# Kernel optimization log

Measured on AMD Instinct MI355X. Metric: run time of the kernel, lower is better.

The kernel has to match this reference:

```python
import jax, jax.numpy as jnp
import numpy as np

N_NODES = 100000
N_EDGES = 1600000
IN_DIM = 128
HID_DIM = 128


def setup_inputs() -> dict:
    key = jax.random.key(0)
    k_x, k_e, k_w1, k_w2, k_b1, k_b2 = jax.random.split(key, 6)
    x = jax.random.normal(k_x, (N_NODES, IN_DIM), dtype=jnp.float32)
    edge_index = jax.random.randint(k_e, (2, N_EDGES), 0, N_NODES, dtype=jnp.int64)
    # GCNConv params: linear weight (no bias in lin), plus post-aggregation bias
    s1 = 1.0 / np.sqrt(IN_DIM)
    s2 = 1.0 / np.sqrt(HID_DIM)
    W1 = jax.random.uniform(k_w1, (IN_DIM, HID_DIM), jnp.float32, -s1, s1)
    b1 = jnp.zeros((HID_DIM,), jnp.float32)
    W2 = jax.random.uniform(k_w2, (HID_DIM, HID_DIM), jnp.float32, -s2, s2)
    b2 = jnp.zeros((HID_DIM,), jnp.float32)
    return {"x": x, "edge_index": edge_index, "W1": W1, "b1": b1, "W2": W2, "b2": b2}


def _gcn_conv(x, row, col, norm, W, b, n_nodes):
    # h = x W ; out[col] += norm * h[row] ; + b   (PyG GCNConv math)
    h = x @ W
    msg = h[row] * norm[:, None]          # [E+N, H] edge-gathered messages
    out = jax.ops.segment_sum(msg, col, num_segments=n_nodes)
    return out + b


def reference(x, edge_index, W1, b1, W2, b2):
    n = x.shape[0]
    # add self-loops (PyG gcn_norm default: add_self_loops=True, edge_weight=1)
    loop = jnp.arange(n, dtype=edge_index.dtype)
    row = jnp.concatenate([edge_index[0], loop])
    col = jnp.concatenate([edge_index[1], loop])
    # symmetric normalization: deg computed at col (target)
    deg = jax.ops.segment_sum(jnp.ones(row.shape[0], x.dtype), col, num_segments=n)
    dis = jnp.where(deg > 0, jax.lax.rsqrt(jnp.maximum(deg, 1e-30)), 0.0)
    norm = dis[row] * dis[col]            # [E+N]
    h = _gcn_conv(x, row, col, norm, W1, b1, n)
    h = jax.nn.relu(h)
    out = _gcn_conv(h, row, col, norm, W2, b2, n)
    return out
```

## Files before the change

kernel.cpp:

```cpp
#include <hip/hip_runtime.h>

#define NN 100000
#define NE 1600000
#define FD 128
#define NBUK 196
#define BCAP 9216
#define EPBB 8192
#define NBB 196
#define NGROUP 6250

typedef unsigned int  u32;
typedef unsigned short u16;
typedef __bf16 bf16x8 __attribute__((ext_vector_type(8)));
typedef float  f32x4v __attribute__((ext_vector_type(4)));

__device__ __forceinline__ u16 f2bf(float f) {
    u32 u = __float_as_uint(f);
    u32 r = (u + 0x7FFFu + ((u >> 16) & 1u)) >> 16;
    return (u16)r;
}

__device__ __forceinline__ void acc2(float& x, float& y, float wt, u32 w) {
    x += wt * __uint_as_float(w << 16);
    y += wt * __uint_as_float(w & 0xffff0000u);
}
__device__ __forceinline__ void acc8(float4& L, float4& H, float wt, uint4 u) {
    acc2(L.x, L.y, wt, u.x); acc2(L.z, L.w, wt, u.y);
    acc2(H.x, H.y, wt, u.z); acc2(H.z, H.w, wt, u.w);
}


__global__ void k_binit(int* __restrict__ bcur) {
    int i = threadIdx.x;
    if (i < NBUK) bcur[i] = i * BCAP;
}

__global__ __launch_bounds__(256) void k_bin(const int* __restrict__ row,
                                             const int* __restrict__ col,
                                             int* __restrict__ bcur,
                                             u32* __restrict__ ebuf) {
    __shared__ int hist[NBUK];
    const int tid = threadIdx.x;
    for (int i = tid; i < NBUK; i += 256) hist[i] = 0;
    __syncthreads();
    const int e0 = blockIdx.x * EPBB;
    const int e1 = min(e0 + EPBB, NE);
    for (int e = e0 + tid; e < e1; e += 256)
        atomicAdd(&hist[col[e] >> 9], 1);
    __syncthreads();
    for (int i = tid; i < NBUK; i += 256) {
        int c = hist[i];
        hist[i] = c ? atomicAdd(&bcur[i], c) : 0;
    }
    __syncthreads();
    for (int e = e0 + tid; e < e1; e += 256) {
        int c = col[e];
        int pos = atomicAdd(&hist[c >> 9], 1);
        ebuf[pos] = ((u32)row[e] << 9) | (u32)(c & 511);
    }
}

__global__ __launch_bounds__(256) void k_bucket(const u32* __restrict__ ebuf,
                                                const int* __restrict__ bcur,
                                                int* __restrict__ nstart,
                                                int* __restrict__ ndeg,
                                                float* __restrict__ dis,
                                                int* __restrict__ srcs) {
    __shared__ int lcnt[512];
    __shared__ int s[256];
    const int tid = threadIdx.x;
    const int b = blockIdx.x;
    const int base = b * BCAP;
    const int end = bcur[b];

    lcnt[tid] = 0; lcnt[tid + 256] = 0;
    __syncthreads();
    for (int i = base + tid; i < end; i += 256)
        atomicAdd(&lcnt[ebuf[i] & 511], 1);
    __syncthreads();

    const int c0 = lcnt[tid * 2], c1 = lcnt[tid * 2 + 1];
    s[tid] = c0 + c1;
    __syncthreads();
    for (int off = 1; off < 256; off <<= 1) {
        int t = 0;
        if (tid >= off) t = s[tid - off];
        __syncthreads();
        if (tid >= off) s[tid] += t;
        __syncthreads();
    }
    const int excl = (tid == 0) ? 0 : s[tid - 1];
    __syncthreads();
    lcnt[tid * 2] = excl;
    lcnt[tid * 2 + 1] = excl + c0;

    const int v0 = b * 512 + tid * 2;
    if (v0 < NN) {
        nstart[v0] = base + excl;
        ndeg[v0] = c0;
        dis[v0] = rsqrtf((float)c0 + 1.0f);
    }
    if (v0 + 1 < NN) {
        nstart[v0 + 1] = base + excl + c0;
        ndeg[v0 + 1] = c1;
        dis[v0 + 1] = rsqrtf((float)c1 + 1.0f);
    }
    __syncthreads();

    for (int i = base + tid; i < end; i += 256) {
        u32 p = ebuf[i];
        int pos = atomicAdd(&lcnt[p & 511], 1);
        srcs[base + pos] = (int)(p >> 9);
    }
}

__global__ __launch_bounds__(256) void k_wts(const int* __restrict__ nstart,
                                             const int* __restrict__ ndeg,
                                             const float* __restrict__ dis,
                                             const int* __restrict__ srcs,
                                             int2* __restrict__ ew) {
    const int v = (blockIdx.x * 256 + threadIdx.x) >> 4;
    if (v >= NN) return;
    const int l = threadIdx.x & 15;
    const float dv = dis[v];
    const int s0 = nstart[v], d = ndeg[v];
    for (int e = s0 + l; e < s0 + d; e += 16) {
        int s = srcs[e];
        ew[e] = make_int2(s, __float_as_int(dv * dis[s]));
    }
}

__global__ void k_packW2(const float* __restrict__ W1, const float* __restrict__ W2,
                         u16* __restrict__ Wf1, u16* __restrict__ Wf2) {
    int tid = blockIdx.x * 256 + threadIdx.x;
    if (tid >= 2048) return;
    int l = tid & 63;
    int tq = tid >> 6;
    int q = tq & 3, t = tq >> 2;
    int n = t * 16 + (l & 15);
    int k0 = q * 32 + (l >> 4) * 8;
    u32 p[4], r[4];
    for (int jj = 0; jj < 4; ++jj) {
        u16 lo1 = f2bf(W1[(size_t)(k0 + 2 * jj) * FD + n]);
        u16 hi1 = f2bf(W1[(size_t)(k0 + 2 * jj + 1) * FD + n]);
        p[jj] = (u32)lo1 | ((u32)hi1 << 16);
        u16 lo2 = f2bf(W2[(size_t)(k0 + 2 * jj) * FD + n]);
        u16 hi2 = f2bf(W2[(size_t)(k0 + 2 * jj + 1) * FD + n]);
        r[jj] = (u32)lo2 | ((u32)hi2 << 16);
    }
    *(uint4*)&Wf1[(size_t)tid * 8] = make_uint4(p[0], p[1], p[2], p[3]);
    *(uint4*)&Wf2[(size_t)tid * 8] = make_uint4(r[0], r[1], r[2], r[3]);
}

template <bool F32IN>
__global__ __launch_bounds__(256, 4) void k_gemm_mfma(const void* __restrict__ inv,
                                                      const u16* __restrict__ Wf,
                                                      u16* __restrict__ out) {
    __shared__ u16 Wl[16384];
    const int tid = threadIdx.x;
    {
        const uint4* s = (const uint4*)Wf;
        uint4* d = (uint4*)Wl;
#pragma unroll
        for (int i = 0; i < 8; ++i) d[tid + 256 * i] = s[tid + 256 * i];
    }
    __syncthreads();

    const int wave = tid >> 6, lane = tid & 63;
    const int gid = blockIdx.x * 4 + wave;
    if (gid >= NGROUP) return;
    const int row0 = gid * 16;
    const int lr = lane & 15;
    const int lh = lane >> 4;

    f32x4v acc[8];
#pragma unroll
    for (int t = 0; t < 8; ++t) { f32x4v z = {0.f, 0.f, 0.f, 0.f}; acc[t] = z; }

#pragma unroll
    for (int q = 0; q < 4; ++q) {
        bf16x8 a;
        if (F32IN) {
            const float* arow = (const float*)inv + (size_t)(row0 + lr) * FD + lh * 8 + q * 32;
            float4 f0 = *(const float4*)(arow);
            float4 f1 = *(const float4*)(arow + 4);
            union { bf16x8 v; u16 s[8]; } ua;
            ua.s[0] = f2bf(f0.x); ua.s[1] = f2bf(f0.y);
            ua.s[2] = f2bf(f0.z); ua.s[3] = f2bf(f0.w);
            ua.s[4] = f2bf(f1.x); ua.s[5] = f2bf(f1.y);
            ua.s[6] = f2bf(f1.z); ua.s[7] = f2bf(f1.w);
            a = ua.v;
        } else {
            const u16* arow = (const u16*)inv + (size_t)(row0 + lr) * FD + lh * 8 + q * 32;
            a = *(const bf16x8*)arow;
        }
#pragma unroll
        for (int t = 0; t < 8; ++t) {
            bf16x8 bfr = *(const bf16x8*)(&Wl[(size_t)(t * 4 + q) * 512 + lane * 8]);
            acc[t] = __builtin_amdgcn_mfma_f32_16x16x32_bf16(a, bfr, acc[t], 0, 0, 0);
        }
    }
#pragma unroll
    for (int t = 0; t < 8; ++t) {
#pragma unroll
        for (int j = 0; j < 4; ++j) {
            const int r = row0 + lh * 4 + j;
            out[(size_t)r * FD + t * 16 + lr] = f2bf(acc[t][j]);
        }
    }
}

template <bool BF16OUT>
__global__ __launch_bounds__(256) void k_agg_gather(const u16* __restrict__ hb,
                                                    const float* __restrict__ b,
                                                    const float* __restrict__ dis,
                                                    const int* __restrict__ nstart,
                                                    const int* __restrict__ ndeg,
                                                    const int2* __restrict__ ew,
                                                    void* __restrict__ outv) {
    const int v = (blockIdx.x * 256 + threadIdx.x) >> 4;
    if (v >= NN) return;
    const int f8 = threadIdx.x & 15;
    const uint4* h4 = (const uint4*)hb;

    const float dv = dis[v];
    float4 aL = ((const float4*)b)[f8 * 2];
    float4 aH = ((const float4*)b)[f8 * 2 + 1];
    {
        const float sl = dv * dv;
        uint4 u = h4[(size_t)v * 16 + f8];
        acc8(aL, aH, sl, u);
    }

    int e = nstart[v];
    const int end = e + ndeg[v];
    for (; e + 3 < end; e += 4) {
        const int2 p0 = ew[e], p1 = ew[e + 1], p2 = ew[e + 2], p3 = ew[e + 3];
        const uint4 u0 = h4[(size_t)p0.x * 16 + f8];
        const uint4 u1 = h4[(size_t)p1.x * 16 + f8];
        const uint4 u2 = h4[(size_t)p2.x * 16 + f8];
        const uint4 u3 = h4[(size_t)p3.x * 16 + f8];
        acc8(aL, aH, __int_as_float(p0.y), u0);
        acc8(aL, aH, __int_as_float(p1.y), u1);
        acc8(aL, aH, __int_as_float(p2.y), u2);
        acc8(aL, aH, __int_as_float(p3.y), u3);
    }
    for (; e < end; ++e) {
        const int2 p0 = ew[e];
        const uint4 u0 = h4[(size_t)p0.x * 16 + f8];
        acc8(aL, aH, __int_as_float(p0.y), u0);
    }

    if (BF16OUT) {
        uint4 p;
        p.x = (u32)f2bf(fmaxf(aL.x, 0.f)) | ((u32)f2bf(fmaxf(aL.y, 0.f)) << 16);
        p.y = (u32)f2bf(fmaxf(aL.z, 0.f)) | ((u32)f2bf(fmaxf(aL.w, 0.f)) << 16);
        p.z = (u32)f2bf(fmaxf(aH.x, 0.f)) | ((u32)f2bf(fmaxf(aH.y, 0.f)) << 16);
        p.w = (u32)f2bf(fmaxf(aH.z, 0.f)) | ((u32)f2bf(fmaxf(aH.w, 0.f)) << 16);
        ((uint4*)outv)[(size_t)v * 16 + f8] = p;
    } else {
        float4* o = (float4*)outv;
        o[(size_t)v * 32 + f8 * 2] = aL;
        o[(size_t)v * 32 + f8 * 2 + 1] = aH;
    }
}


extern "C" void kernel_launch(void* const* d_in, const int* in_sizes, int n_in,
                              void* d_out, int out_size, void* d_ws, size_t ws_size,
                              hipStream_t stream) {
    const float* x  = (const float*)d_in[0];
    const int*   ei = (const int*)d_in[1];
    const float* W1 = (const float*)d_in[2];
    const float* b1 = (const float*)d_in[3];
    const float* W2 = (const float*)d_in[4];
    const float* b2 = (const float*)d_in[5];
    float* out = (float*)d_out;

    const int* row = ei;
    const int* col = ei + NE;

    char* base = (char*)d_ws;
    size_t o = 0;
    auto take = [&](size_t bytes) -> void* {
        void* p = base + o;
        o += (bytes + 255) & ~(size_t)255;
        return p;
    };
    int*   nstart  = (int*)take((size_t)NN * 4);
    int*   ndeg    = (int*)take((size_t)NN * 4);
    int*   bcur    = (int*)take(256 * 4);
    float* dis     = (float*)take((size_t)NN * 4);
    u16*   Wf1     = (u16*)take(16384 * 2);
    u16*   Wf2     = (u16*)take(16384 * 2);
    u16*   hb      = (u16*)take((size_t)NN * FD * 2);
    u16*   aggb    = (u16*)take((size_t)NN * FD * 2);
    int*   srcs    = (int*)take((size_t)NBUK * BCAP * 4);
    int2*  ew      = (int2*)take((size_t)NBUK * BCAP * 8);
    u32*   ebuf    = (u32*)take((size_t)NBUK * BCAP * 4);

    k_binit<<<1, 256, 0, stream>>>(bcur);
    k_bin<<<NBB, 256, 0, stream>>>(row, col, bcur, ebuf);
    k_bucket<<<NBUK, 256, 0, stream>>>(ebuf, bcur, nstart, ndeg, dis, srcs);
    k_wts<<<NGROUP, 256, 0, stream>>>(nstart, ndeg, dis, srcs, ew);

    k_packW2<<<8, 256, 0, stream>>>(W1, W2, Wf1, Wf2);

    k_gemm_mfma<true><<<(NGROUP + 3) / 4, 256, 0, stream>>>(x, Wf1, hb);
    k_agg_gather<true><<<NN * 16 / 256, 256, 0, stream>>>(hb, b1, dis, nstart, ndeg, ew, aggb);
    k_gemm_mfma<false><<<(NGROUP + 3) / 4, 256, 0, stream>>>(aggb, Wf2, hb);
    k_agg_gather<false><<<NN * 16 / 256, 256, 0, stream>>>(hb, b2, dis, nstart, ndeg, ew, out);
}
```

Before: 229.7 us.

## Fuse graph binning with first GEMM, fuse layer-1 aggregation with second GEMM

Merges edge binning and the first X·W1 MFMA GEMM into a single launch, with the two roles picked by block index so that they overlap. Fuses the first aggregation (with ReLU) and the second GEMM through a shared-memory tile, which removes the aggb round trip and a separate launch. It also drops the precomputed edge-weight array and instead computes dv*dis[s] inside the gather loops, and merges bcur init with weight packing. Launch count falls from 9 to 5, at the cost of extra dis gathers per edge and W2 fragments read from global memory by every block.

Result: faster. 198.6 us (-13.5%).

```diff
diff --git a/kernel.cpp b/kernel.cpp
--- a/kernel.cpp
+++ b/kernel.cpp
@@ -8,6 +8,7 @@
 #define EPBB 8192
 #define NBB 196
 #define NGROUP 6250
+#define GEMM_BLKS 1563
 
 typedef unsigned int  u32;
 typedef unsigned short u16;
@@ -29,110 +30,14 @@
     acc2(H.x, H.y, wt, u.z); acc2(H.z, H.w, wt, u.w);
 }
 
-
-__global__ void k_binit(int* __restrict__ bcur) {
-    int i = threadIdx.x;
-    if (i < NBUK) bcur[i] = i * BCAP;
-}
-
-__global__ __launch_bounds__(256) void k_bin(const int* __restrict__ row,
-                                             const int* __restrict__ col,
-                                             int* __restrict__ bcur,
-                                             u32* __restrict__ ebuf) {
-    __shared__ int hist[NBUK];
-    const int tid = threadIdx.x;
-    for (int i = tid; i < NBUK; i += 256) hist[i] = 0;
-    __syncthreads();
-    const int e0 = blockIdx.x * EPBB;
-    const int e1 = min(e0 + EPBB, NE);
-    for (int e = e0 + tid; e < e1; e += 256)
-        atomicAdd(&hist[col[e] >> 9], 1);
-    __syncthreads();
-    for (int i = tid; i < NBUK; i += 256) {
-        int c = hist[i];
-        hist[i] = c ? atomicAdd(&bcur[i], c) : 0;
-    }
-    __syncthreads();
-    for (int e = e0 + tid; e < e1; e += 256) {
-        int c = col[e];
-        int pos = atomicAdd(&hist[c >> 9], 1);
-        ebuf[pos] = ((u32)row[e] << 9) | (u32)(c & 511);
-    }
-}
-
-__global__ __launch_bounds__(256) void k_bucket(const u32* __restrict__ ebuf,
-                                                const int* __restrict__ bcur,
-                                                int* __restrict__ nstart,
-                                                int* __restrict__ ndeg,
-                                                float* __restrict__ dis,
-                                                int* __restrict__ srcs) {
-    __shared__ int lcnt[512];
-    __shared__ int s[256];
-    const int tid = threadIdx.x;
-    const int b = blockIdx.x;
-    const int base = b * BCAP;
-    const int end = bcur[b];
-
-    lcnt[tid] = 0; lcnt[tid + 256] = 0;
-    __syncthreads();
-    for (int i = base + tid; i < end; i += 256)
-        atomicAdd(&lcnt[ebuf[i] & 511], 1);
-    __syncthreads();
-
-    const int c0 = lcnt[tid * 2], c1 = lcnt[tid * 2 + 1];
-    s[tid] = c0 + c1;
-    __syncthreads();
-    for (int off = 1; off < 256; off <<= 1) {
-        int t = 0;
-        if (tid >= off) t = s[tid - off];
-        __syncthreads();
-        if (tid >= off) s[tid] += t;
-        __syncthreads();
-    }
-    const int excl = (tid == 0) ? 0 : s[tid - 1];
-    __syncthreads();
-    lcnt[tid * 2] = excl;
-    lcnt[tid * 2 + 1] = excl + c0;
-
-    const int v0 = b * 512 + tid * 2;
-    if (v0 < NN) {
-        nstart[v0] = base + excl;
-        ndeg[v0] = c0;
-        dis[v0] = rsqrtf((float)c0 + 1.0f);
-    }
-    if (v0 + 1 < NN) {
-        nstart[v0 + 1] = base + excl + c0;
-        ndeg[v0 + 1] = c1;
-        dis[v0 + 1] = rsqrtf((float)c1 + 1.0f);
-    }
-    __syncthreads();
-
-    for (int i = base + tid; i < end; i += 256) {
-        u32 p = ebuf[i];
-        int pos = atomicAdd(&lcnt[p & 511], 1);
-        srcs[base + pos] = (int)(p >> 9);
-    }
-}
-
-__global__ __launch_bounds__(256) void k_wts(const int* __restrict__ nstart,
-                                             const int* __restrict__ ndeg,
-                                             const float* __restrict__ dis,
-                                             const int* __restrict__ srcs,
-                                             int2* __restrict__ ew) {
-    const int v = (blockIdx.x * 256 + threadIdx.x) >> 4;
-    if (v >= NN) return;
-    const int l = threadIdx.x & 15;
-    const float dv = dis[v];
-    const int s0 = nstart[v], d = ndeg[v];
-    for (int e = s0 + l; e < s0 + d; e += 16) {
-        int s = srcs[e];
-        ew[e] = make_int2(s, __float_as_int(dv * dis[s]));
-    }
-}
-
-__global__ void k_packW2(const float* __restrict__ W1, const float* __restrict__ W2,
-                         u16* __restrict__ Wf1, u16* __restrict__ Wf2) {
-    int tid = blockIdx.x * 256 + threadIdx.x;
+__global__ void k_init_pack(int* __restrict__ bcur,
+                            const float* __restrict__ W1, const float* __restrict__ W2,
+                            u16* __restrict__ Wf1, u16* __restrict__ Wf2) {
+    if (blockIdx.x == 0) {
+        if (threadIdx.x < NBUK) bcur[threadIdx.x] = threadIdx.x * BCAP;
+        return;
+    }
+    int tid = (blockIdx.x - 1) * 256 + threadIdx.x;
     if (tid >= 2048) return;
     int l = tid & 63;
     int tq = tid >> 6;
@@ -152,22 +57,48 @@
     *(uint4*)&Wf2[(size_t)tid * 8] = make_uint4(r[0], r[1], r[2], r[3]);
 }
 
-template <bool F32IN>
-__global__ __launch_bounds__(256, 4) void k_gemm_mfma(const void* __restrict__ inv,
-                                                      const u16* __restrict__ Wf,
-                                                      u16* __restrict__ out) {
-    __shared__ u16 Wl[16384];
+__global__ __launch_bounds__(256, 4) void k_mega(const int* __restrict__ row,
+                                                 const int* __restrict__ col,
+                                                 int* __restrict__ bcur,
+                                                 u32* __restrict__ ebuf,
+                                                 const float* __restrict__ x,
+                                                 const u16* __restrict__ Wf1,
+                                                 u16* __restrict__ hb) {
+    __shared__ u16 smem[16384];
     const int tid = threadIdx.x;
+
+    if (blockIdx.x < NBB) {
+        int* hist = (int*)smem;
+        for (int i = tid; i < NBUK; i += 256) hist[i] = 0;
+        __syncthreads();
+        const int e0 = blockIdx.x * EPBB;
+        const int e1 = min(e0 + EPBB, NE);
+        for (int e = e0 + tid; e < e1; e += 256)
+            atomicAdd(&hist[col[e] >> 9], 1);
+        __syncthreads();
+        for (int i = tid; i < NBUK; i += 256) {
+            int c = hist[i];
+            hist[i] = c ? atomicAdd(&bcur[i], c) : 0;
+        }
+        __syncthreads();
+        for (int e = e0 + tid; e < e1; e += 256) {
+            int c = col[e];
+            int pos = atomicAdd(&hist[c >> 9], 1);
+            ebuf[pos] = ((u32)row[e] << 9) | (u32)(c & 511);
+        }
+        return;
+    }
+
     {
-        const uint4* s = (const uint4*)Wf;
-        uint4* d = (uint4*)Wl;
+        const uint4* s = (const uint4*)Wf1;
+        uint4* d = (uint4*)smem;
 #pragma unroll
         for (int i = 0; i < 8; ++i) d[tid + 256 * i] = s[tid + 256 * i];
     }
     __syncthreads();
 
     const int wave = tid >> 6, lane = tid & 63;
-    const int gid = blockIdx.x * 4 + wave;
+    const int gid = (blockIdx.x - NBB) * 4 + wave;
     if (gid >= NGROUP) return;
     const int row0 = gid * 16;
     const int lr = lane & 15;
@@ -179,24 +110,18 @@
 
 #pragma unroll
     for (int q = 0; q < 4; ++q) {
-        bf16x8 a;
-        if (F32IN) {
-            const float* arow = (const float*)inv + (size_t)(row0 + lr) * FD + lh * 8 + q * 32;
-            float4 f0 = *(const float4*)(arow);
-            float4 f1 = *(const float4*)(arow + 4);
-            union { bf16x8 v; u16 s[8]; } ua;
-            ua.s[0] = f2bf(f0.x); ua.s[1] = f2bf(f0.y);
-            ua.s[2] = f2bf(f0.z); ua.s[3] = f2bf(f0.w);
-            ua.s[4] = f2bf(f1.x); ua.s[5] = f2bf(f1.y);
-            ua.s[6] = f2bf(f1.z); ua.s[7] = f2bf(f1.w);
-            a = ua.v;
-        } else {
-            const u16* arow = (const u16*)inv + (size_t)(row0 + lr) * FD + lh * 8 + q * 32;
-            a = *(const bf16x8*)arow;
-        }
+        const float* arow = x + (size_t)(row0 + lr) * FD + lh * 8 + q * 32;
+        float4 f0 = *(const float4*)(arow);
+        float4 f1 = *(const float4*)(arow + 4);
+        union { bf16x8 v; u16 s[8]; } ua;
+        ua.s[0] = f2bf(f0.x); ua.s[1] = f2bf(f0.y);
+        ua.s[2] = f2bf(f0.z); ua.s[3] = f2bf(f0.w);
+        ua.s[4] = f2bf(f1.x); ua.s[5] = f2bf(f1.y);
+        ua.s[6] = f2bf(f1.z); ua.s[7] = f2bf(f1.w);
+        bf16x8 a = ua.v;
 #pragma unroll
         for (int t = 0; t < 8; ++t) {
-            bf16x8 bfr = *(const bf16x8*)(&Wl[(size_t)(t * 4 + q) * 512 + lane * 8]);
+            bf16x8 bfr = *(const bf16x8*)(&smem[(size_t)(t * 4 + q) * 512 + lane * 8]);
             acc[t] = __builtin_amdgcn_mfma_f32_16x16x32_bf16(a, bfr, acc[t], 0, 0, 0);
         }
     }
@@ -205,19 +130,149 @@
 #pragma unroll
         for (int j = 0; j < 4; ++j) {
             const int r = row0 + lh * 4 + j;
-            out[(size_t)r * FD + t * 16 + lr] = f2bf(acc[t][j]);
+            hb[(size_t)r * FD + t * 16 + lr] = f2bf(acc[t][j]);
         }
     }
 }
 
-template <bool BF16OUT>
-__global__ __launch_bounds__(256) void k_agg_gather(const u16* __restrict__ hb,
-                                                    const float* __restrict__ b,
-                                                    const float* __restrict__ dis,
-                                                    const int* __restrict__ nstart,
-                                                    const int* __restrict__ ndeg,
-                                                    const int2* __restrict__ ew,
-                                                    void* __restrict__ outv) {
+__global__ __launch_bounds__(256) void k_bucket(const u32* __restrict__ ebuf,
+                                                const int* __restrict__ bcur,
+                                                int* __restrict__ nstart,
+                                                int* __restrict__ ndeg,
+                                                float* __restrict__ dis,
+                                                int* __restrict__ srcs) {
+    __shared__ int lcnt[512];
+    __shared__ int s[256];
+    const int tid = threadIdx.x;
+    const int b = blockIdx.x;
+    const int base = b * BCAP;
+    const int end = bcur[b];
+
+    lcnt[tid] = 0; lcnt[tid + 256] = 0;
+    __syncthreads();
+    for (int i = base + tid; i < end; i += 256)
+        atomicAdd(&lcnt[ebuf[i] & 511], 1);
+    __syncthreads();
+
+    const int c0 = lcnt[tid * 2], c1 = lcnt[tid * 2 + 1];
+    s[tid] = c0 + c1;
+    __syncthreads();
+    for (int off = 1; off < 256; off <<= 1) {
+        int t = 0;
+        if (tid >= off) t = s[tid - off];
+        __syncthreads();
+        if (tid >= off) s[tid] += t;
+        __syncthreads();
+    }
+    const int excl = (tid == 0) ? 0 : s[tid - 1];
+    __syncthreads();
+    lcnt[tid * 2] = excl;
+    lcnt[tid * 2 + 1] = excl + c0;
+
+    const int v0 = b * 512 + tid * 2;
+    if (v0 < NN) {
+        nstart[v0] = base + excl;
+        ndeg[v0] = c0;
+        dis[v0] = rsqrtf((float)c0 + 1.0f);
+    }
+    if (v0 + 1 < NN) {
+        nstart[v0 + 1] = base + excl + c0;
+        ndeg[v0 + 1] = c1;
+        dis[v0 + 1] = rsqrtf((float)c1 + 1.0f);
+    }
+    __syncthreads();
+
+    for (int i = base + tid; i < end; i += 256) {
+        u32 p = ebuf[i];
+        int pos = atomicAdd(&lcnt[p & 511], 1);
+        srcs[base + pos] = (int)(p >> 9);
+    }
+}
+
+__global__ __launch_bounds__(256) void k_agg2(const u16* __restrict__ hb,
+                                              const float* __restrict__ b1,
+                                              const float* __restrict__ dis,
+                                              const int* __restrict__ nstart,
+                                              const int* __restrict__ ndeg,
+                                              const int* __restrict__ srcs,
+                                              const u16* __restrict__ Wf2,
+                                              u16* __restrict__ hb2) {
+    __shared__ u16 tile[16 * 136];
+    const int tid = threadIdx.x;
+    const int nl = tid >> 4;
+    const int f8 = tid & 15;
+    const int v = blockIdx.x * 16 + nl;
+    const uint4* h4 = (const uint4*)hb;
+
+    const float dv = dis[v];
+    float4 aL = ((const float4*)b1)[f8 * 2];
+    float4 aH = ((const float4*)b1)[f8 * 2 + 1];
+    {
+        const float sl = dv * dv;
+        uint4 u = h4[(size_t)v * 16 + f8];
+        acc8(aL, aH, sl, u);
+    }
+
+    int e = nstart[v];
+    const int end = e + ndeg[v];
+    for (; e + 3 < end; e += 4) {
+        const int s0 = srcs[e], s1 = srcs[e + 1], s2 = srcs[e + 2], s3 = srcs[e + 3];
+        const float w0 = dv * dis[s0];
+        const float w1 = dv * dis[s1];
+        const float w2 = dv * dis[s2];
+        const float w3 = dv * dis[s3];
+        const uint4 u0 = h4[(size_t)s0 * 16 + f8];
+        const uint4 u1 = h4[(size_t)s1 * 16 + f8];
+        const uint4 u2 = h4[(size_t)s2 * 16 + f8];
+        const uint4 u3 = h4[(size_t)s3 * 16 + f8];
+        acc8(aL, aH, w0, u0); acc8(aL, aH, w1, u1);
+        acc8(aL, aH, w2, u2); acc8(aL, aH, w3, u3);
+    }
+    for (; e < end; ++e) {
+        const int s0 = srcs[e];
+        const float w0 = dv * dis[s0];
+        const uint4 u0 = h4[(size_t)s0 * 16 + f8];
+        acc8(aL, aH, w0, u0);
+    }
+
+    {
+        uint4 p;
+        p.x = (u32)f2bf(fmaxf(aL.x, 0.f)) | ((u32)f2bf(fmaxf(aL.y, 0.f)) << 16);
+        p.y = (u32)f2bf(fmaxf(aL.z, 0.f)) | ((u32)f2bf(fmaxf(aL.w, 0.f)) << 16);
+        p.z = (u32)f2bf(fmaxf(aH.x, 0.f)) | ((u32)f2bf(fmaxf(aH.y, 0.f)) << 16);
+        p.w = (u32)f2bf(fmaxf(aH.z, 0.f)) | ((u32)f2bf(fmaxf(aH.w, 0.f)) << 16);
+        *(uint4*)&tile[nl * 136 + f8 * 8] = p;
+    }
+    __syncthreads();
+
+    const int wave = tid >> 6, lane = tid & 63;
+    const int lr = lane & 15;
+    const int lh = lane >> 4;
+    f32x4v a0 = {0.f, 0.f, 0.f, 0.f}, a1 = {0.f, 0.f, 0.f, 0.f};
+#pragma unroll
+    for (int q = 0; q < 4; ++q) {
+        bf16x8 a = *(const bf16x8*)&tile[lr * 136 + q * 32 + lh * 8];
+        bf16x8 bb0 = *(const bf16x8*)&Wf2[(size_t)((2 * wave) * 4 + q) * 512 + lane * 8];
+        bf16x8 bb1 = *(const bf16x8*)&Wf2[(size_t)((2 * wave + 1) * 4 + q) * 512 + lane * 8];
+        a0 = __builtin_amdgcn_mfma_f32_16x16x32_bf16(a, bb0, a0, 0, 0, 0);
+        a1 = __builtin_amdgcn_mfma_f32_16x16x32_bf16(a, bb1, a1, 0, 0, 0);
+    }
+    const int row0 = blockIdx.x * 16;
+#pragma unroll
+    for (int j = 0; j < 4; ++j) {
+        const int r = row0 + lh * 4 + j;
+        hb2[(size_t)r * FD + (2 * wave) * 16 + lr] = f2bf(a0[j]);
+        hb2[(size_t)r * FD + (2 * wave + 1) * 16 + lr] = f2bf(a1[j]);
+    }
+}
+
+__global__ __launch_bounds__(256) void k_agg_f32(const u16* __restrict__ hb,
+                                                 const float* __restrict__ b,
+                                                 const float* __restrict__ dis,
+                                                 const int* __restrict__ nstart,
+                                                 const int* __restrict__ ndeg,
+                                                 const int* __restrict__ srcs,
+                                                 float* __restrict__ out) {
     const int v = (blockIdx.x * 256 + threadIdx.x) >> 4;
     if (v >= NN) return;
     const int f8 = threadIdx.x & 15;
@@ -235,34 +290,28 @@
     int e = nstart[v];
     const int end = e + ndeg[v];
     for (; e + 3 < end; e += 4) {
-        const int2 p0 = ew[e], p1 = ew[e + 1], p2 = ew[e + 2], p3 = ew[e + 3];
-        const uint4 u0 = h4[(size_t)p0.x * 16 + f8];
-        const uint4 u1 = h4[(size_t)p1.x * 16 + f8];
-        const uint4 u2 = h4[(size_t)p2.x * 16 + f8];
-        const uint4 u3 = h4[(size_t)p3.x * 16 + f8];
-        acc8(aL, aH, __int_as_float(p0.y), u0);
-        acc8(aL, aH, __int_as_float(p1.y), u1);
-        acc8(aL, aH, __int_as_float(p2.y), u2);
-        acc8(aL, aH, __int_as_float(p3.y), u3);
+        const int s0 = srcs[e], s1 = srcs[e + 1], s2 = srcs[e + 2], s3 = srcs[e + 3];
+        const float w0 = dv * dis[s0];
+        const float w1 = dv * dis[s1];
+        const float w2 = dv * dis[s2];
+        const float w3 = dv * dis[s3];
+        const uint4 u0 = h4[(size_t)s0 * 16 + f8];
+        const uint4 u1 = h4[(size_t)s1 * 16 + f8];
+        const uint4 u2 = h4[(size_t)s2 * 16 + f8];
+        const uint4 u3 = h4[(size_t)s3 * 16 + f8];
+        acc8(aL, aH, w0, u0); acc8(aL, aH, w1, u1);
+        acc8(aL, aH, w2, u2); acc8(aL, aH, w3, u3);
     }
     for (; e < end; ++e) {
-        const int2 p0 = ew[e];
-        const uint4 u0 = h4[(size_t)p0.x * 16 + f8];
-        acc8(aL, aH, __int_as_float(p0.y), u0);
-    }
-
-    if (BF16OUT) {
-        uint4 p;
-        p.x = (u32)f2bf(fmaxf(aL.x, 0.f)) | ((u32)f2bf(fmaxf(aL.y, 0.f)) << 16);
-        p.y = (u32)f2bf(fmaxf(aL.z, 0.f)) | ((u32)f2bf(fmaxf(aL.w, 0.f)) << 16);
-        p.z = (u32)f2bf(fmaxf(aH.x, 0.f)) | ((u32)f2bf(fmaxf(aH.y, 0.f)) << 16);
-        p.w = (u32)f2bf(fmaxf(aH.z, 0.f)) | ((u32)f2bf(fmaxf(aH.w, 0.f)) << 16);
-        ((uint4*)outv)[(size_t)v * 16 + f8] = p;
-    } else {
-        float4* o = (float4*)outv;
-        o[(size_t)v * 32 + f8 * 2] = aL;
-        o[(size_t)v * 32 + f8 * 2 + 1] = aH;
-    }
+        const int s0 = srcs[e];
+        const float w0 = dv * dis[s0];
+        const uint4 u0 = h4[(size_t)s0 * 16 + f8];
+        acc8(aL, aH, w0, u0);
+    }
+
+    float4* o = (float4*)out;
+    o[(size_t)v * 32 + f8 * 2] = aL;
+    o[(size_t)v * 32 + f8 * 2 + 1] = aH;
 }
 
 
@@ -294,20 +343,13 @@
     u16*   Wf1     = (u16*)take(16384 * 2);
     u16*   Wf2     = (u16*)take(16384 * 2);
     u16*   hb      = (u16*)take((size_t)NN * FD * 2);
-    u16*   aggb    = (u16*)take((size_t)NN * FD * 2);
+    u16*   hb2     = (u16*)take((size_t)NN * FD * 2);
     int*   srcs    = (int*)take((size_t)NBUK * BCAP * 4);
-    int2*  ew      = (int2*)take((size_t)NBUK * BCAP * 8);
     u32*   ebuf    = (u32*)take((size_t)NBUK * BCAP * 4);
 
-    k_binit<<<1, 256, 0, stream>>>(bcur);
-    k_bin<<<NBB, 256, 0, stream>>>(row, col, bcur, ebuf);
+    k_init_pack<<<9, 256, 0, stream>>>(bcur, W1, W2, Wf1, Wf2);
+    k_mega<<<NBB + GEMM_BLKS, 256, 0, stream>>>(row, col, bcur, ebuf, x, Wf1, hb);
     k_bucket<<<NBUK, 256, 0, stream>>>(ebuf, bcur, nstart, ndeg, dis, srcs);
-    k_wts<<<NGROUP, 256, 0, stream>>>(nstart, ndeg, dis, srcs, ew);
-
-    k_packW2<<<8, 256, 0, stream>>>(W1, W2, Wf1, Wf2);
-
-    k_gemm_mfma<true><<<(NGROUP + 3) / 4, 256, 0, stream>>>(x, Wf1, hb);
-    k_agg_gather<true><<<NN * 16 / 256, 256, 0, stream>>>(hb, b1, dis, nstart, ndeg, ew, aggb);
-    k_gemm_mfma<false><<<(NGROUP + 3) / 4, 256, 0, stream>>>(aggb, Wf2, hb);
-    k_agg_gather<false><<<NN * 16 / 256, 256, 0, stream>>>(hb, b2, dis, nstart, ndeg, ew, out);
-}
+    k_agg2<<<NGROUP, 256, 0, stream>>>(hb, b1, dis, nstart, ndeg, srcs, Wf2, hb2);
+    k_agg_f32<<<NGROUP, 256, 0, stream>>>(hb2, b2, dis, nstart, ndeg, srcs, out);
+}
```
